# Performance work log

Measured on AMD Instinct MI355X. Metric: run time of the kernel, lower is better.

The kernel has to match this reference:

```python
import jax, jax.numpy as jnp
import numpy as np

D_MODEL = 1024
D_INNER = 2048      # expand * d_model
D_STATE = 64
HEADDIM = 128
NHEADS = 16         # d_inner // headdim
D_CONV = 4
CHUNK = 256
D_IN_PROJ = 2 * D_INNER + 2 * D_STATE + NHEADS   # 4240 (ngroups=1)
CONV_DIM = D_INNER + 2 * D_STATE                 # 2176
EPS = 1e-5


def setup_inputs() -> dict:
    key = jax.random.key(0)
    ks = jax.random.split(key, 8)
    B, L = 2, 4096
    u = jax.random.normal(ks[0], (B, L, D_MODEL), jnp.float32)
    in_proj_w = jax.random.normal(ks[1], (D_IN_PROJ, D_MODEL), jnp.float32) / np.sqrt(D_MODEL)
    conv_w = jax.random.uniform(ks[2], (CONV_DIM, D_CONV), jnp.float32, -0.5, 0.5)
    conv_b = jnp.zeros((CONV_DIM,), jnp.float32)
    # dt_bias init exactly as in the module: inv-softplus of dt ~ logU(1e-3, 1e-1)
    dt0 = jnp.exp(jax.random.uniform(ks[3], (NHEADS,), jnp.float32) * (np.log(0.1) - np.log(0.001)) + np.log(0.001))
    dt_bias = dt0 + jnp.log(-jnp.expm1(-dt0))
    A_log = jnp.log(jax.random.uniform(ks[4], (NHEADS,), jnp.float32, 1.0, 16.0))
    Dp = jnp.ones((NHEADS,), jnp.float32)
    norm_w = jnp.ones((D_INNER,), jnp.float32)
    out_proj_w = jax.random.normal(ks[5], (D_MODEL, D_INNER), jnp.float32) / np.sqrt(D_INNER)
    return dict(u=u, in_proj_w=in_proj_w, conv_w=conv_w, conv_b=conv_b, dt_bias=dt_bias,
                A_log=A_log, Dp=Dp, norm_w=norm_w, out_proj_w=out_proj_w)


def _ssd(x, dt, A, Bm, Cm, Dp):
    # Chunked selective state-space scan (mamba_chunk_scan_combined semantics).
    # x: [b,l,h,p], dt: [b,l,h] (already softplus'd), A: [h] (negative), Bm/Cm: [b,l,n]
    b, l, h, p = x.shape
    n = Bm.shape[-1]
    nc = l // CHUNK
    xc = x.reshape(b, nc, CHUNK, h, p)
    dtc = dt.reshape(b, nc, CHUNK, h)
    Bc = Bm.reshape(b, nc, CHUNK, n)
    Cc = Cm.reshape(b, nc, CHUNK, n)
    a = dtc * A                       # [b,c,q,h], a <= 0
    acum = jnp.cumsum(a, axis=2)      # within-chunk cumulative log-decay
    # ---- intra-chunk (causal, attention-like) ----
    scores = jnp.einsum('bcqn,bckn->bcqk', Cc, Bc)
    diff = acum[:, :, :, None, :] - acum[:, :, None, :, :]        # [b,c,q,k,h]
    mask = jnp.tril(jnp.ones((CHUNK, CHUNK), bool))[None, None, :, :, None]
    decay = jnp.exp(jnp.where(mask, diff, -jnp.inf))
    M = scores[..., None] * decay * dtc[:, :, None, :, :]         # [b,c,q,k,h]
    y_diag = jnp.einsum('bcqkh,bckhp->bcqhp', M, xc)
    # ---- per-chunk end states ----
    decay_states = jnp.exp(acum[:, :, -1:, :] - acum)             # [b,c,q,h]
    states = jnp.einsum('bcqh,bcqn,bcqhp->bchpn', dtc * decay_states, Bc, xc)
    # ---- inter-chunk recurrence (scan over nc chunks) ----
    chunk_decay = jnp.exp(acum[:, :, -1, :])                      # [b,c,h]
    def step(s, inp):
        st, cd = inp
        return cd[:, :, None, None] * s + st, s                   # emit state BEFORE this chunk
    init = jnp.zeros((b, h, p, n), x.dtype)
    _, prev = jax.lax.scan(step, init, (states.transpose(1, 0, 2, 3, 4), chunk_decay.transpose(1, 0, 2)))
    prev = prev.transpose(1, 0, 2, 3, 4)                          # [b,c,h,p,n]
    y_off = jnp.einsum('bcqn,bchpn,bcqh->bcqhp', Cc, prev, jnp.exp(acum))
    y = y_diag + y_off + xc * Dp[None, None, None, :, None]
    return y.reshape(b, l, h, p)


def _forward(u, in_proj_w, conv_w, conv_b, dt_bias, A_log, Dp, norm_w, out_proj_w):
    b, l, _ = u.shape
    zxbct = jnp.einsum('bld,ed->ble', u, in_proj_w)
    z = zxbct[..., :D_INNER]
    xBC = zxbct[..., D_INNER:D_INNER + CONV_DIM]
    dt = zxbct[..., D_INNER + CONV_DIM:]
    dt = jax.nn.softplus(dt + dt_bias)                            # [b,l,h]
    # causal depthwise conv1d (padding d_conv-1, truncated to seq_len) + SiLU
    xp = jnp.pad(xBC, ((0, 0), (D_CONV - 1, 0), (0, 0)))
    conv_out = conv_b
    for w in range(D_CONV):
        conv_out = conv_out + xp[:, w:w + l, :] * conv_w[:, w]
    xBC = jax.nn.silu(conv_out)
    x = xBC[..., :D_INNER]
    Bm = xBC[..., D_INNER:D_INNER + D_STATE]
    Cm = xBC[..., D_INNER + D_STATE:]
    A = -jnp.exp(A_log)
    y = _ssd(x.reshape(b, l, NHEADS, HEADDIM), dt, A, Bm, Cm, Dp)
    y = y.reshape(b, l, D_INNER)
    # RMSNormGated (norm_before_gate=False): gate first, then RMSNorm
    y = y * jax.nn.silu(z)
    y = y * jax.lax.rsqrt(jnp.mean(y * y, axis=-1, keepdims=True) + EPS) * norm_w
    return jnp.einsum('ble,de->bld', y, out_proj_w)


def reference(u, in_proj_w, conv_w, conv_b, dt_bias, A_log, Dp, norm_w, out_proj_w):
    return _forward(u, in_proj_w, conv_w, conv_b, dt_bias, A_log, Dp, norm_w, out_proj_w)
```

## Files before the change

kernel.cpp:

```cpp
#include <hip/hip_runtime.h>
#include <hip/hip_bf16.h>
#include <cstdint>
#include <cstddef>

#define D_MODEL   1024
#define D_INNER   2048
#define D_STATE   64
#define HEADDIM   128
#define NHEADS    16
#define D_CONV    4
#define CHUNK     256
#define D_IN_PROJ 4240
#define ZPAD      4352
#define CONV_DIM  2176
#define NB        2
#define LEN       4096
#define NC        16
#define MROWS     (NB*LEN)

typedef __hip_bfloat16 bf16;
typedef __bf16 bf16x8 __attribute__((ext_vector_type(8)));
typedef float  f32x4  __attribute__((ext_vector_type(4)));
typedef unsigned short us4 __attribute__((ext_vector_type(4)));

__device__ __forceinline__ float fsilu(float x){ return x / (1.f + __expf(-x)); }
__device__ __forceinline__ float toF(float x){ return x; }
__device__ __forceinline__ float toF(bf16 x){ return __bfloat162float(x); }
__device__ __forceinline__ void storeF(float* p, float v){ *p = v; }
__device__ __forceinline__ void storeF(bf16* p, float v){ *p = __float2bfloat16(v); }

__device__ __forceinline__ unsigned short f2bs(float v){
  return __bfloat16_as_ushort(__float2bfloat16(v));
}
__device__ __forceinline__ void store4(bf16* p, f32x4 v){
  us4 o; o[0]=f2bs(v[0]); o[1]=f2bs(v[1]); o[2]=f2bs(v[2]); o[3]=f2bs(v[3]);
  *(us4*)p = o;
}
__device__ __forceinline__ void store4(float* p, f32x4 v){
  *(f32x4*)p = v;
}

__device__ __forceinline__ void gload_lds16(const void* g, void* l){
  __builtin_amdgcn_global_load_lds(
     (const __attribute__((address_space(1))) unsigned int*)(uintptr_t)g,
     (__attribute__((address_space(3))) unsigned int*)(uintptr_t)l, 16, 0, 0);
}

template<typename TC>
__global__ __launch_bounds__(256) void k_gemm_mfma(
    const bf16* __restrict__ A, int lda,
    const bf16* __restrict__ B, int ldb,
    TC* __restrict__ C, int ldc, int K)
{
  __shared__ __align__(16) bf16 As[128*32];
  __shared__ __align__(16) bf16 Bs[128*32];
  const int tid = threadIdx.x;
  const int w = tid >> 6, l = tid & 63;
  const int quad = l >> 4, lq = l & 15;
  const int m0 = blockIdx.x*128, n0 = blockIdx.y*128;
  const int wm = (w & 1)*64, wn = (w >> 1)*64;
  f32x4 acc[4][4] = {};
  const int sr = l >> 2;
  const int sc = (l & 3)*8;

  for (int k0 = 0; k0 < K; k0 += 32) {
    #pragma unroll
    for (int j = 0; j < 2; j++) {
      const int blk = w*2 + j;
      const int row = blk*16 + sr;
      gload_lds16(A + (size_t)(m0+row)*lda + k0 + sc, (char*)As + blk*1024);
      gload_lds16(B + (size_t)(n0+row)*ldb + k0 + sc, (char*)Bs + blk*1024);
    }
    asm volatile("s_waitcnt vmcnt(0)" ::: "memory");
    __syncthreads();

    const int kq = quad*8;
    const int rA = wm + lq;
    const int rB = wn + lq;
    bf16x8 af[4], bfr[4];
    #pragma unroll
    for (int t = 0; t < 4; t++){
      af[t]  = *(const bf16x8*)&As[(rA + t*16)*32 + kq];
      bfr[t] = *(const bf16x8*)&Bs[(rB + t*16)*32 + kq];
    }
    #pragma unroll
    for (int tm = 0; tm < 4; tm++)
      #pragma unroll
      for (int tn = 0; tn < 4; tn++)
        acc[tm][tn] = __builtin_amdgcn_mfma_f32_16x16x32_bf16(bfr[tn], af[tm], acc[tm][tn], 0,0,0);
    __syncthreads();
  }

  #pragma unroll
  for (int tm = 0; tm < 4; tm++){
    int r = m0 + wm + tm*16 + lq;
    #pragma unroll
    for (int tn = 0; tn < 4; tn++){
      int cb = n0 + wn + tn*16 + quad*4;
      store4(&C[(size_t)r*ldc + cb], acc[tm][tn]);
    }
  }
}

__global__ __launch_bounds__(256) void k_tobf16(
    const float* __restrict__ src, bf16* __restrict__ dst, int n){
  int i = blockIdx.x*256 + threadIdx.x;
  if (i < n) dst[i] = __float2bfloat16(src[i]);
}

__global__ __launch_bounds__(256) void k_padW(
    const float* __restrict__ W, bf16* __restrict__ Wb){
  int i = blockIdx.x*256 + threadIdx.x;
  int r = i >> 10;
  Wb[i] = __float2bfloat16((r < D_IN_PROJ) ? W[i] : 0.f);
}

__global__ __launch_bounds__(256) void k_dt(
    const bf16* __restrict__ zxbct, const float* __restrict__ dt_bias,
    const float* __restrict__ A_log, float* __restrict__ dt_t,
    float* __restrict__ acum_t, float* __restrict__ cd_t){
  int bid = blockIdx.x;
  int h = bid & 15, c = (bid>>4)&15, b = bid>>8;
  int q = threadIdx.x;
  size_t m = (size_t)(b*NC + c)*CHUNK + q;
  float x = toF(zxbct[m*ZPAD + (D_INNER + CONV_DIM) + h]) + dt_bias[h];
  float dtv = (x > 20.f) ? x : log1pf(__expf(x));
  float Ah = -__expf(A_log[h]);
  float a = dtv * Ah;
  __shared__ float sb[CHUNK];
  sb[q] = a;
  __syncthreads();
  #pragma unroll
  for (int off=1; off<CHUNK; off<<=1){
    float t = (q >= off) ? sb[q-off] : 0.f;
    __syncthreads();
    sb[q] += t;
    __syncthreads();
  }
  float ac = sb[q];
  size_t o = ((size_t)(b*NHEADS+h))*LEN + c*CHUNK + q;
  dt_t[o]   = dtv;
  acum_t[o] = ac;
  if (q == CHUNK-1) cd_t[(b*NHEADS+h)*NC + c] = __expf(ac);
}

__global__ __launch_bounds__(256) void k_conv(
    const bf16* __restrict__ zxbct, const float* __restrict__ conv_w,
    const float* __restrict__ conv_b, bf16* __restrict__ xbc){
  __shared__ __align__(16) __bf16 xs[35*64];
  __shared__ __align__(16) float  ws[64*4];
  __shared__ float bs[64];
  const int tid = threadIdx.x;
  const int cq = tid & 7;
  const int tm = tid >> 3;
  const int c0 = blockIdx.x*64;
  const int m0 = blockIdx.y*32;
  {
    int g = m0 - 3 + tm; if (g < 0) g = 0;
    *(bf16x8*)&xs[tm*64 + cq*8] =
        *(const bf16x8*)(zxbct + (size_t)g*ZPAD + D_INNER + c0 + cq*8);
    if (tid < 24){
      int r2 = 32 + (tid >> 3);
      int g2 = m0 - 3 + r2;
      *(bf16x8*)&xs[r2*64 + cq*8] =
          *(const bf16x8*)(zxbct + (size_t)g2*ZPAD + D_INNER + c0 + cq*8);
    }
  }
  if (tid < 64)      *(float4*)&ws[tid*4] = *(const float4*)(conv_w + (size_t)(c0+tid)*4);
  else if (tid < 128) bs[tid-64] = conv_b[c0 + tid - 64];
  __syncthreads();

  const int m = m0 + tm;
  const int l = m & (LEN-1);
  float acc[8];
  #pragma unroll
  for (int j=0;j<8;j++) acc[j] = bs[cq*8+j];
  #pragma unroll
  for (int w=0; w<D_CONV; w++){
    if (l - (D_CONV-1) + w >= 0){
      bf16x8 v = *(const bf16x8*)&xs[(tm+w)*64 + cq*8];
      #pragma unroll
      for (int j=0;j<8;j++) acc[j] += (float)v[j] * ws[(cq*8+j)*4 + w];
    }
  }
  bf16x8 o;
  #pragma unroll
  for (int j=0;j<8;j++) o[j] = (__bf16)fsilu(acc[j]);
  *(bf16x8*)(xbc + (size_t)m*CONV_DIM + c0 + cq*8) = o;
}

__global__ __launch_bounds__(256,2) void k_fused(
    const bf16* __restrict__ xbc, const float* __restrict__ acum_t,
    const float* __restrict__ dt_t, const float* __restrict__ Dp,
    bf16* __restrict__ y, float* __restrict__ states)
{
  const int bid = blockIdx.x;
  const int h = bid & 15, c = (bid>>4)&15, b = bid>>8;
  const int z = b*NC + c;
  const int tid = threadIdx.x;
  const int w = tid >> 6, l = tid & 63;
  const int quad = l >> 4, lq = l & 15;

  __shared__ __align__(16) __bf16 xsT[128*72];
  __shared__ __align__(16) __bf16 bts[64*72];
  __shared__ __align__(16) __bf16 Ms[4][32*40];
  __shared__ float acs[CHUNK], dts[CHUNK];

  const float* acum = acum_t + ((size_t)(b*NHEADS+h))*LEN + c*CHUNK;
  const float* dtc  = dt_t   + ((size_t)(b*NHEADS+h))*LEN + c*CHUNK;
  const float alast = acum[CHUNK-1];
  acs[tid] = acum[tid];
  dts[tid] = dtc[tid];

  const bf16* xrow = xbc + (size_t)z*CHUNK*CONV_DIM + h*HEADDIM;
  const bf16* Brow = xbc + (size_t)z*CHUNK*CONV_DIM + D_INNER;
  const bf16* Crow = xbc + (size_t)z*CHUNK*CONV_DIM + D_INNER + D_STATE;
  const float Dph = Dp[h];
  const int j0 = w, j1 = 7 - w;

  f32x4 Yacc[2][2][8] = {};
  f32x4 Sst[2][4]  = {};

  for (int t = 0; t < 4; t++){
    const int k0 = t*64;
    __syncthreads();
    {
      const bf16* xr = xrow + (size_t)(k0+l)*CONV_DIM;
      #pragma unroll
      for (int pass=0; pass<4; pass++){
        int pb = w*8 + pass*32;
        bf16x8 v = *(const bf16x8*)(xr + pb);
        #pragma unroll
        for (int j=0;j<8;j++) xsT[(pb+j)*72 + l] = v[j];
      }
      float wl = dts[k0+l] * __expf(alast - acs[k0+l]);
      const bf16* br = Brow + (size_t)(k0+l)*CONV_DIM;
      #pragma unroll
      for (int pass=0; pass<2; pass++){
        int nb = w*8 + pass*32;
        bf16x8 v = *(const bf16x8*)(br + nb);
        #pragma unroll
        for (int j=0;j<8;j++) bts[(nb+j)*72 + l] = (__bf16)((float)v[j] * wl);
      }
    }
    __syncthreads();

    #pragma unroll
    for (int s=0;s<2;s++){
      bf16x8 a2[2];
      #pragma unroll
      for (int mi=0;mi<2;mi++)
        a2[mi] = *(const bf16x8*)&xsT[(w*32 + mi*16 + lq)*72 + s*32 + quad*8];
      #pragma unroll
      for (int ni=0;ni<4;ni++){
        bf16x8 bb = *(const bf16x8*)&bts[(ni*16+lq)*72 + s*32 + quad*8];
        #pragma unroll
        for (int mi=0;mi<2;mi++)
          Sst[mi][ni] = __builtin_amdgcn_mfma_f32_16x16x32_bf16(bb, a2[mi], Sst[mi][ni], 0,0,0);
      }
    }

    #pragma unroll
    for (int half=0; half<2; half++){
      const int j = half ? j1 : j0;
      const int qbase = j*32;
      #pragma unroll
      for (int kk=0; kk<2; kk++){
        const int kh = 2*t + kk;
        if (kh > j) continue;
        const int kb32  = kk*32;
        const int kbase = kh*32;
        f32x4 Sacc[2][2] = {};
        #pragma unroll
        for (int s=0;s<2;s++){
          bf16x8 cf[2], bfk[2];
          #pragma unroll
          for (int qm=0;qm<2;qm++)
            cf[qm] = *(const bf16x8*)(Crow + (size_t)(qbase+qm*16+lq)*CONV_DIM + s*32 + quad*8);
          #pragma unroll
          for (int kn=0;kn<2;kn++)
            bfk[kn] = *(const bf16x8*)(Brow + (size_t)(kbase+kn*16+lq)*CONV_DIM + s*32 + quad*8);
          #pragma unroll
          for (int kn=0;kn<2;kn++)
            #pragma unroll
            for (int qm=0;qm<2;qm++)
              Sacc[kn][qm] = __builtin_amdgcn_mfma_f32_16x16x32_bf16(bfk[kn], cf[qm], Sacc[kn][qm], 0,0,0);
        }
        #pragma unroll
        for (int qm=0;qm<2;qm++){
          int ql = qbase + qm*16 + lq;
          float aq = acs[ql];
          #pragma unroll
          for (int kn=0;kn<2;kn++){
            us4 o;
            #pragma unroll
            for (int i=0;i<4;i++){
              int kl = kbase + kn*16 + quad*4 + i;
              float v = Sacc[kn][qm][i] * __expf(aq - acs[kl]) * dts[kl];
              v = (kl < ql) ? v : ((kl == ql) ? v + Dph : 0.f);
              o[i] = f2bs(v);
            }
            *(us4*)&Ms[w][(qm*16+lq)*40 + kn*16 + quad*4] = o;
          }
        }
        asm volatile("s_waitcnt lgkmcnt(0)" ::: "memory");
        #pragma unroll
        for (int qm=0;qm<2;qm++){
          bf16x8 am = *(const bf16x8*)&Ms[w][(qm*16+lq)*40 + quad*8];
          #pragma unroll
          for (int pn=0;pn<8;pn++){
            bf16x8 bp = *(const bf16x8*)&xsT[(pn*16+lq)*72 + kb32 + quad*8];
            Yacc[half][qm][pn] = __builtin_amdgcn_mfma_f32_16x16x32_bf16(bp, am, Yacc[half][qm][pn], 0,0,0);
          }
        }
      }
    }
  }

  bf16* yrow = y + (size_t)z*CHUNK*D_INNER + h*HEADDIM;
  #pragma unroll
  for (int half=0; half<2; half++){
    const int j = half ? j1 : j0;
    #pragma unroll
    for (int qm=0;qm<2;qm++){
      int q = j*32 + qm*16 + lq;
      #pragma unroll
      for (int pn=0;pn<8;pn++)
        store4(&yrow[(size_t)q*D_INNER + pn*16 + quad*4], Yacc[half][qm][pn]);
    }
  }
  float* so = states + (size_t)bid*HEADDIM*D_STATE;
  #pragma unroll
  for (int mi=0;mi<2;mi++){
    int pp = w*32 + mi*16 + lq;
    #pragma unroll
    for (int ni=0;ni<4;ni++)
      store4(&so[pp*D_STATE + ni*16 + quad*4], Sst[mi][ni]);
  }
}

__global__ __launch_bounds__(256) void k_scan(
    const float* __restrict__ states, const float* __restrict__ cd_t,
    bf16* __restrict__ prevb){
  int b = blockIdx.x >> 4, h = blockIdx.x & 15;
  int pt = blockIdx.y;
  int tid = threadIdx.x;
  float carry[4] = {0.f,0.f,0.f,0.f};
  for (int c=0;c<NC;c++){
    size_t base = ((size_t)(b*256 + c*16 + h))*HEADDIM*D_STATE + (size_t)pt*1024;
    float cd = cd_t[(b*NHEADS+h)*NC + c];
    #pragma unroll
    for (int i=0;i<4;i++){
      size_t idx = base + (size_t)i*256 + tid;
      prevb[idx] = __float2bfloat16(carry[i]);
      carry[i] = carry[i]*cd + states[idx];
    }
  }
}

__global__ __launch_bounds__(256,2) void k_yoff(
    const bf16* __restrict__ xbc, const bf16* __restrict__ prevb,
    const float* __restrict__ acum_t, bf16* __restrict__ y){
  const int bid = blockIdx.x;
  const int h = bid & 15, c = (bid>>4)&15, b = bid>>8;
  const int z = b*NC + c;
  const int tid = threadIdx.x;
  const int w = tid >> 6, l = tid & 63;
  const int quad = l >> 4, lq = l & 15;
  const bf16* Crow = xbc + (size_t)z*CHUNK*CONV_DIM + D_INNER + D_STATE;
  const bf16* pv = prevb + (size_t)bid*HEADDIM*D_STATE;
  const float* acum = acum_t + ((size_t)(b*NHEADS+h))*LEN + c*CHUNK;
  const int qw = w*64;
  f32x4 acc[4][8] = {};
  #pragma unroll
  for (int s=0;s<2;s++){
    bf16x8 bp[8];
    #pragma unroll
    for (int pn=0;pn<8;pn++)
      bp[pn] = *(const bf16x8*)(pv + (pn*16+lq)*D_STATE + s*32 + quad*8);
    #pragma unroll
    for (int qm=0;qm<4;qm++){
      int row = qw + qm*16 + lq;
      float e = __expf(acum[row]);
      bf16x8 a = *(const bf16x8*)(Crow + (size_t)row*CONV_DIM + s*32 + quad*8);
      bf16x8 ae;
      #pragma unroll
      for (int j=0;j<8;j++) ae[j] = (__bf16)((float)a[j] * e);
      #pragma unroll
      for (int pn=0;pn<8;pn++)
        acc[qm][pn] = __builtin_amdgcn_mfma_f32_16x16x32_bf16(bp[pn], ae, acc[qm][pn], 0,0,0);
    }
  }
  bf16* yrow = y + (size_t)z*CHUNK*D_INNER + h*HEADDIM;
  #pragma unroll
  for (int qm=0;qm<4;qm++){
    int q = qw + qm*16 + lq;
    #pragma unroll
    for (int pn=0;pn<8;pn++){
      bf16* yp = &yrow[(size_t)q*D_INNER + pn*16 + quad*4];
      us4 old = *(const us4*)yp;
      us4 o;
      #pragma unroll
      for (int i=0;i<4;i++)
        o[i] = f2bs(__bfloat162float(__ushort_as_bfloat16(old[i])) + acc[qm][pn][i]);
      *(us4*)yp = o;
    }
  }
}

__global__ __launch_bounds__(256) void k_gatenorm(
    const bf16* __restrict__ zxbct, const float* __restrict__ norm_w,
    bf16* __restrict__ y){
  int m = blockIdx.x;
  int e0 = threadIdx.x*8;
  bf16x8 zv = *(const bf16x8*)(zxbct + (size_t)m*ZPAD + e0);
  bf16x8 yv = *(const bf16x8*)(y + (size_t)m*D_INNER + e0);
  float4 nw0 = *(const float4*)(norm_w + e0);
  float4 nw1 = *(const float4*)(norm_w + e0 + 4);
  float v[8]; float ss = 0.f;
  #pragma unroll
  for (int j=0;j<8;j++){
    float val = (float)yv[j] * fsilu((float)zv[j]);
    v[j] = val; ss += val*val;
  }
  #pragma unroll
  for (int off=32; off>0; off>>=1) ss += __shfl_down(ss, off, 64);
  __shared__ float red[4];
  if ((threadIdx.x & 63) == 0) red[threadIdx.x >> 6] = ss;
  __syncthreads();
  float tot = red[0]+red[1]+red[2]+red[3];
  float r = rsqrtf(tot * (1.f/D_INNER) + 1e-5f);
  float nw[8] = {nw0.x,nw0.y,nw0.z,nw0.w,nw1.x,nw1.y,nw1.z,nw1.w};
  bf16x8 o;
  #pragma unroll
  for (int j=0;j<8;j++) o[j] = (__bf16)(v[j] * r * nw[j]);
  *(bf16x8*)(y + (size_t)m*D_INNER + e0) = o;
}

extern "C" void kernel_launch(void* const* d_in, const int* in_sizes, int n_in,
                              void* d_out, int out_size, void* d_ws, size_t ws_size,
                              hipStream_t stream) {
  const float* u         = (const float*)d_in[0];
  const float* in_proj_w = (const float*)d_in[1];
  const float* conv_w    = (const float*)d_in[2];
  const float* conv_b    = (const float*)d_in[3];
  const float* dt_bias   = (const float*)d_in[4];
  const float* A_log     = (const float*)d_in[5];
  const float* Dp        = (const float*)d_in[6];
  const float* norm_w    = (const float*)d_in[7];
  const float* out_proj_w= (const float*)d_in[8];
  float* out = (float*)d_out;

  char* p = (char*)d_ws;
  auto alloc = [&](size_t bytes){ char* r = p; p += (bytes + 255) & ~size_t(255); return r; };
  bf16*  zxbct = (bf16*) alloc((size_t)MROWS*ZPAD*2);
  bf16*  xbc   = (bf16*) alloc((size_t)MROWS*CONV_DIM*2);
  bf16*  y     = (bf16*) alloc((size_t)MROWS*D_INNER*2);
  bf16*  ub    = (bf16*) alloc((size_t)MROWS*D_MODEL*2);
  bf16*  Wb_in = (bf16*) alloc((size_t)ZPAD*D_MODEL*2);
  bf16*  Wb_out= (bf16*) alloc((size_t)D_MODEL*D_INNER*2);
  float* dt_t  = (float*)alloc((size_t)NB*NHEADS*LEN*4);
  float* acum_t= (float*)alloc((size_t)NB*NHEADS*LEN*4);
  float* cd_t  = (float*)alloc((size_t)NB*NHEADS*NC*4);
  float* states= (float*)ub;
  bf16*  prevb = (bf16*)Wb_in;

  dim3 blk(256);
  k_tobf16<<<dim3((MROWS*D_MODEL+255)/256), blk, 0, stream>>>(u, ub, MROWS*D_MODEL);
  k_padW  <<<dim3((ZPAD*D_MODEL)/256), blk, 0, stream>>>(in_proj_w, Wb_in);
  k_tobf16<<<dim3((D_MODEL*D_INNER+255)/256), blk, 0, stream>>>(out_proj_w, Wb_out, D_MODEL*D_INNER);

  k_gemm_mfma<bf16><<<dim3(MROWS/128, ZPAD/128), blk, 0, stream>>>(
      ub, D_MODEL, Wb_in, D_MODEL, zxbct, ZPAD, D_MODEL);

  k_dt   <<<dim3(NB*NC*NHEADS), blk, 0, stream>>>(zxbct, dt_bias, A_log, dt_t, acum_t, cd_t);
  k_conv <<<dim3(CONV_DIM/64, MROWS/32), blk, 0, stream>>>(zxbct, conv_w, conv_b, xbc);
  k_fused<<<dim3(NB*NC*NHEADS), blk, 0, stream>>>(xbc, acum_t, dt_t, Dp, y, states);
  k_scan <<<dim3(NB*NHEADS, 8), blk, 0, stream>>>(states, cd_t, prevb);
  k_yoff <<<dim3(NB*NC*NHEADS), blk, 0, stream>>>(xbc, prevb, acum_t, y);
  k_gatenorm<<<dim3(MROWS), blk, 0, stream>>>(zxbct, norm_w, y);

  k_gemm_mfma<float><<<dim3(MROWS/128, D_MODEL/128), blk, 0, stream>>>(
      y, D_INNER, Wb_out, D_INNER, out, D_MODEL, D_INNER);
}
```

Baseline: 423.0 us.

## Fuse conversion kernels, fold norm weight into out_proj, widen GEMM K-step

Merges the three fp32-to-bf16 conversion kernels into one vectorized kernel and folds the RMSNorm weight into the out_proj weight conversion, so the gate-norm kernel no longer reads norm_w. The MFMA GEMM now loads two 32-wide K slices per barrier, halving the number of sync/wait rounds per K loop at the cost of doubled LDS. In the fused SSD kernel, the C fragments are hoisted out of the inner kh loop so they load once per query block, with an early skip when no key block applies. Rounding changes slightly because the norm weight is applied to bf16 weights before the GEMM rather than to activations.

Measured after the change: 376.7 us. 10.9% less time.

```diff
diff --git a/kernel.cpp b/kernel.cpp
--- a/kernel.cpp
+++ b/kernel.cpp
@@ -52,8 +52,8 @@
     const bf16* __restrict__ B, int ldb,
     TC* __restrict__ C, int ldc, int K)
 {
-  __shared__ __align__(16) bf16 As[128*32];
-  __shared__ __align__(16) bf16 Bs[128*32];
+  __shared__ __align__(16) bf16 As[2][128*32];
+  __shared__ __align__(16) bf16 Bs[2][128*32];
   const int tid = threadIdx.x;
   const int w = tid >> 6, l = tid & 63;
   const int quad = l >> 4, lq = l & 15;
@@ -63,31 +63,35 @@
   const int sr = l >> 2;
   const int sc = (l & 3)*8;
 
-  for (int k0 = 0; k0 < K; k0 += 32) {
-    #pragma unroll
-    for (int j = 0; j < 2; j++) {
-      const int blk = w*2 + j;
-      const int row = blk*16 + sr;
-      gload_lds16(A + (size_t)(m0+row)*lda + k0 + sc, (char*)As + blk*1024);
-      gload_lds16(B + (size_t)(n0+row)*ldb + k0 + sc, (char*)Bs + blk*1024);
+  for (int k0 = 0; k0 < K; k0 += 64) {
+    #pragma unroll
+    for (int half = 0; half < 2; half++){
+      #pragma unroll
+      for (int j = 0; j < 2; j++) {
+        const int blk = w*2 + j;
+        const int row = blk*16 + sr;
+        gload_lds16(A + (size_t)(m0+row)*lda + k0 + half*32 + sc, (char*)As[half] + blk*1024);
+        gload_lds16(B + (size_t)(n0+row)*ldb + k0 + half*32 + sc, (char*)Bs[half] + blk*1024);
+      }
     }
     asm volatile("s_waitcnt vmcnt(0)" ::: "memory");
     __syncthreads();
 
     const int kq = quad*8;
-    const int rA = wm + lq;
-    const int rB = wn + lq;
-    bf16x8 af[4], bfr[4];
-    #pragma unroll
-    for (int t = 0; t < 4; t++){
-      af[t]  = *(const bf16x8*)&As[(rA + t*16)*32 + kq];
-      bfr[t] = *(const bf16x8*)&Bs[(rB + t*16)*32 + kq];
-    }
-    #pragma unroll
-    for (int tm = 0; tm < 4; tm++)
-      #pragma unroll
-      for (int tn = 0; tn < 4; tn++)
-        acc[tm][tn] = __builtin_amdgcn_mfma_f32_16x16x32_bf16(bfr[tn], af[tm], acc[tm][tn], 0,0,0);
+    #pragma unroll
+    for (int half = 0; half < 2; half++){
+      bf16x8 af[4], bfr[4];
+      #pragma unroll
+      for (int t = 0; t < 4; t++){
+        af[t]  = *(const bf16x8*)&As[half][(wm + lq + t*16)*32 + kq];
+        bfr[t] = *(const bf16x8*)&Bs[half][(wn + lq + t*16)*32 + kq];
+      }
+      #pragma unroll
+      for (int tm = 0; tm < 4; tm++)
+        #pragma unroll
+        for (int tn = 0; tn < 4; tn++)
+          acc[tm][tn] = __builtin_amdgcn_mfma_f32_16x16x32_bf16(bfr[tn], af[tm], acc[tm][tn], 0,0,0);
+    }
     __syncthreads();
   }
 
@@ -102,17 +106,32 @@
   }
 }
 
-__global__ __launch_bounds__(256) void k_tobf16(
-    const float* __restrict__ src, bf16* __restrict__ dst, int n){
-  int i = blockIdx.x*256 + threadIdx.x;
-  if (i < n) dst[i] = __float2bfloat16(src[i]);
-}
-
-__global__ __launch_bounds__(256) void k_padW(
-    const float* __restrict__ W, bf16* __restrict__ Wb){
-  int i = blockIdx.x*256 + threadIdx.x;
-  int r = i >> 10;
-  Wb[i] = __float2bfloat16((r < D_IN_PROJ) ? W[i] : 0.f);
+#define NU4  (MROWS*D_MODEL/4)
+#define NW14 (ZPAD*D_MODEL/4)
+#define NW24 (D_MODEL*D_INNER/4)
+__global__ __launch_bounds__(256) void k_convert(
+    const float* __restrict__ u, const float* __restrict__ Win,
+    const float* __restrict__ Wout, const float* __restrict__ norm_w,
+    bf16* __restrict__ ub, bf16* __restrict__ Wb_in, bf16* __restrict__ Wb_out){
+  int i4 = blockIdx.x*256 + threadIdx.x;
+  if (i4 < NU4){
+    float4 v = ((const float4*)u)[i4];
+    us4 o = {f2bs(v.x), f2bs(v.y), f2bs(v.z), f2bs(v.w)};
+    ((us4*)ub)[i4] = o;
+  } else if (i4 < NU4 + NW14){
+    int j = i4 - NU4;
+    int r = j >> 8;
+    float4 v = make_float4(0.f,0.f,0.f,0.f);
+    if (r < D_IN_PROJ) v = ((const float4*)Win)[j];
+    us4 o = {f2bs(v.x), f2bs(v.y), f2bs(v.z), f2bs(v.w)};
+    ((us4*)Wb_in)[j] = o;
+  } else {
+    int j = i4 - NU4 - NW14;
+    float4 v = ((const float4*)Wout)[j];
+    float4 nw = ((const float4*)norm_w)[j & 511];
+    us4 o = {f2bs(v.x*nw.x), f2bs(v.y*nw.y), f2bs(v.z*nw.z), f2bs(v.w*nw.w)};
+    ((us4*)Wb_out)[j] = o;
+  }
 }
 
 __global__ __launch_bounds__(256) void k_dt(
@@ -263,7 +282,14 @@
     #pragma unroll
     for (int half=0; half<2; half++){
       const int j = half ? j1 : j0;
+      if (2*t > j) continue;
       const int qbase = j*32;
+      bf16x8 cf[2][2];
+      #pragma unroll
+      for (int s=0;s<2;s++)
+        #pragma unroll
+        for (int qm=0;qm<2;qm++)
+          cf[s][qm] = *(const bf16x8*)(Crow + (size_t)(qbase+qm*16+lq)*CONV_DIM + s*32 + quad*8);
       #pragma unroll
       for (int kk=0; kk<2; kk++){
         const int kh = 2*t + kk;
@@ -273,10 +299,7 @@
         f32x4 Sacc[2][2] = {};
         #pragma unroll
         for (int s=0;s<2;s++){
-          bf16x8 cf[2], bfk[2];
-          #pragma unroll
-          for (int qm=0;qm<2;qm++)
-            cf[qm] = *(const bf16x8*)(Crow + (size_t)(qbase+qm*16+lq)*CONV_DIM + s*32 + quad*8);
+          bf16x8 bfk[2];
           #pragma unroll
           for (int kn=0;kn<2;kn++)
             bfk[kn] = *(const bf16x8*)(Brow + (size_t)(kbase+kn*16+lq)*CONV_DIM + s*32 + quad*8);
@@ -284,7 +307,7 @@
           for (int kn=0;kn<2;kn++)
             #pragma unroll
             for (int qm=0;qm<2;qm++)
-              Sacc[kn][qm] = __builtin_amdgcn_mfma_f32_16x16x32_bf16(bfk[kn], cf[qm], Sacc[kn][qm], 0,0,0);
+              Sacc[kn][qm] = __builtin_amdgcn_mfma_f32_16x16x32_bf16(bfk[kn], cf[s][qm], Sacc[kn][qm], 0,0,0);
         }
         #pragma unroll
         for (int qm=0;qm<2;qm++){
@@ -409,14 +432,11 @@
 }
 
 __global__ __launch_bounds__(256) void k_gatenorm(
-    const bf16* __restrict__ zxbct, const float* __restrict__ norm_w,
-    bf16* __restrict__ y){
+    const bf16* __restrict__ zxbct, bf16* __restrict__ y){
   int m = blockIdx.x;
   int e0 = threadIdx.x*8;
   bf16x8 zv = *(const bf16x8*)(zxbct + (size_t)m*ZPAD + e0);
   bf16x8 yv = *(const bf16x8*)(y + (size_t)m*D_INNER + e0);
-  float4 nw0 = *(const float4*)(norm_w + e0);
-  float4 nw1 = *(const float4*)(norm_w + e0 + 4);
   float v[8]; float ss = 0.f;
   #pragma unroll
   for (int j=0;j<8;j++){
@@ -430,10 +450,9 @@
   __syncthreads();
   float tot = red[0]+red[1]+red[2]+red[3];
   float r = rsqrtf(tot * (1.f/D_INNER) + 1e-5f);
-  float nw[8] = {nw0.x,nw0.y,nw0.z,nw0.w,nw1.x,nw1.y,nw1.z,nw1.w};
   bf16x8 o;
   #pragma unroll
-  for (int j=0;j<8;j++) o[j] = (__bf16)(v[j] * r * nw[j]);
+  for (int j=0;j<8;j++) o[j] = (__bf16)(v[j] * r);
   *(bf16x8*)(y + (size_t)m*D_INNER + e0) = o;
 }
 
@@ -466,9 +485,8 @@
   bf16*  prevb = (bf16*)Wb_in;
 
   dim3 blk(256);
-  k_tobf16<<<dim3((MROWS*D_MODEL+255)/256), blk, 0, stream>>>(u, ub, MROWS*D_MODEL);
-  k_padW  <<<dim3((ZPAD*D_MODEL)/256), blk, 0, stream>>>(in_proj_w, Wb_in);
-  k_tobf16<<<dim3((D_MODEL*D_INNER+255)/256), blk, 0, stream>>>(out_proj_w, Wb_out, D_MODEL*D_INNER);
+  k_convert<<<dim3((NU4+NW14+NW24)/256), blk, 0, stream>>>(
+      u, in_proj_w, out_proj_w, norm_w, ub, Wb_in, Wb_out);
 
   k_gemm_mfma<bf16><<<dim3(MROWS/128, ZPAD/128), blk, 0, stream>>>(
       ub, D_MODEL, Wb_in, D_MODEL, zxbct, ZPAD, D_MODEL);
@@ -478,7 +496,7 @@
   k_fused<<<dim3(NB*NC*NHEADS), blk, 0, stream>>>(xbc, acum_t, dt_t, Dp, y, states);
   k_scan <<<dim3(NB*NHEADS, 8), blk, 0, stream>>>(states, cd_t, prevb);
   k_yoff <<<dim3(NB*NC*NHEADS), blk, 0, stream>>>(xbc, prevb, acum_t, y);
-  k_gatenorm<<<dim3(MROWS), blk, 0, stream>>>(zxbct, norm_w, y);
+  k_gatenorm<<<dim3(MROWS), blk, 0, stream>>>(zxbct, y);
 
   k_gemm_mfma<float><<<dim3(MROWS/128, D_MODEL/128), blk, 0, stream>>>(
       y, D_INNER, Wb_out, D_INNER, out, D_MODEL, D_INNER);
```
